# Optimization experiments

Measured on AMD Instinct MI355X. Metric: run time of the kernel, lower is better.

The kernel has to match this reference:

```python
import jax, jax.numpy as jnp
import numpy as np

N = 100000
E = 1600000
IN_F = 256
OUT_F = 128


def setup_inputs() -> dict:
    key = jax.random.key(0)
    k1, k2, k3, k4 = jax.random.split(key, 4)
    x = jax.random.normal(k1, (N, IN_F), dtype=jnp.float32)
    weight = jax.random.normal(k2, (IN_F, OUT_F), dtype=jnp.float32) / np.sqrt(IN_F)
    bias = jax.random.normal(k3, (OUT_F,), dtype=jnp.float32) * 0.01
    edge_index = jax.random.randint(k4, (2, E), 0, N, dtype=jnp.int32)
    return {"x": x, "weight": weight, "bias": bias, "edge_index": edge_index}


def reference(x, weight, bias, edge_index):
    # support = X @ W  -> [N, out]
    support = jnp.matmul(x, weight)
    row, col = edge_index[0], edge_index[1]
    # scatter-add gathered neighbor features: agg[col] += support[row]
    agg = jax.ops.segment_sum(support[row], col, num_segments=N)
    # self term + bias
    return agg + support + bias
```

## Files before the change

### kernel.cpp

```cpp
#include <hip/hip_runtime.h>

#define NUM_NODES 100000
#define IN_F 256
#define OUT_F 128
#define TILE 128
#define NT ((NUM_NODES + TILE - 1) / TILE)
#define NSG 98
#define CHUNK1 4096
#define CHUNK2 4096
#define CAP1 20480
#define SUB2 (CAP1 / CHUNK2)
#define CAP 2560

typedef __attribute__((ext_vector_type(8))) short bf16x8;
typedef __attribute__((ext_vector_type(4))) float f32x4;

__device__ inline unsigned short f2bf(float f) {
    unsigned u = __float_as_uint(f);
    u = (u + 0x7FFFu + ((u >> 16) & 1u)) >> 16;
    return (unsigned short)u;
}
__device__ inline float bf_lo(unsigned int u) { return __uint_as_float(u << 16); }
__device__ inline float bf_hi(unsigned int u) { return __uint_as_float(u & 0xFFFF0000u); }

__global__ __launch_bounds__(256) void convert_wt_kernel(
    const float* __restrict__ w, unsigned short* __restrict__ wt)
{
    int g = blockIdx.x * 256 + threadIdx.x;
    int k = g >> 7, n = g & 127;
    wt[n * 256 + k] = f2bf(w[g]);
}

__global__ __launch_bounds__(512) void gemm_mfma_kernel(
    const float* __restrict__ x, const unsigned short* __restrict__ wt,
    unsigned short* __restrict__ support_h)
{
    __shared__ unsigned short WT[128][264];

    const int tid = threadIdx.x;
    const uint4* src = reinterpret_cast<const uint4*>(wt);
#pragma unroll
    for (int i = 0; i < 8; ++i) {
        int j = tid + i * 512;
        int r = j >> 5;
        int c = (j & 31) << 3;
        *reinterpret_cast<uint4*>(&WT[r][c]) = src[j];
    }
    __syncthreads();

    const int wave = tid >> 6;
    const int lane = tid & 63;
    const int q = lane >> 4;
    const int r16 = lane & 15;
    const int strip_row = blockIdx.x * 128 + wave * 16;

    int arow = strip_row + r16;
    if (arow >= NUM_NODES) arow = NUM_NODES - 1;
    const float* xrow = x + (size_t)arow * IN_F + q * 8;

    f32x4 acc[8];
#pragma unroll
    for (int n = 0; n < 8; ++n) acc[n] = (f32x4){0.f, 0.f, 0.f, 0.f};

#pragma unroll
    for (int half = 0; half < 2; ++half) {
        float4 a[8];
#pragma unroll
        for (int g = 0; g < 4; ++g) {
            const float* p = xrow + half * 128 + g * 32;
            a[g * 2]     = *reinterpret_cast<const float4*>(p);
            a[g * 2 + 1] = *reinterpret_cast<const float4*>(p + 4);
        }
#pragma unroll
        for (int g = 0; g < 4; ++g) {
            const int k0 = half * 128 + g * 32;
            bf16x8 af;
            af[0] = (short)f2bf(a[g * 2].x);
            af[1] = (short)f2bf(a[g * 2].y);
            af[2] = (short)f2bf(a[g * 2].z);
            af[3] = (short)f2bf(a[g * 2].w);
            af[4] = (short)f2bf(a[g * 2 + 1].x);
            af[5] = (short)f2bf(a[g * 2 + 1].y);
            af[6] = (short)f2bf(a[g * 2 + 1].z);
            af[7] = (short)f2bf(a[g * 2 + 1].w);
#pragma unroll
            for (int n = 0; n < 8; ++n) {
                bf16x8 bfr = *reinterpret_cast<const bf16x8*>(
                    &WT[n * 16 + r16][k0 + q * 8]);
                acc[n] = __builtin_amdgcn_mfma_f32_16x16x32_bf16(
                    af, bfr, acc[n], 0, 0, 0);
            }
        }
    }

#pragma unroll
    for (int n = 0; n < 8; ++n) {
#pragma unroll
        for (int rr = 0; rr < 4; ++rr) {
            int grow = strip_row + q * 4 + rr;
            if (grow < NUM_NODES)
                support_h[(size_t)grow * OUT_F + n * 16 + r16] = f2bf(acc[n][rr]);
        }
    }
}

__global__ __launch_bounds__(256) void sg_split_kernel(
    const int* __restrict__ ei, int E, int* __restrict__ gcur1,
    unsigned int* __restrict__ g1rec)
{
    __shared__ int hist[NSG], base[NSG], gbase[NSG], cur[NSG];
    __shared__ unsigned int sorted[CHUNK1];
    const int t = threadIdx.x;
    const int e0 = blockIdx.x * CHUNK1;

    for (int i = t; i < NSG; i += 256) hist[i] = 0;
    __syncthreads();

#pragma unroll
    for (int i = 0; i < CHUNK1 / 256; ++i) {
        int e = e0 + i * 256 + t;
        if (e < E) atomicAdd(&hist[ei[E + e] >> 10], 1);
    }
    __syncthreads();

    {
        int* scan = (int*)sorted;
        const int i0 = t * 4;
        int v0 = (i0     < NSG) ? hist[i0]     : 0;
        int v1 = (i0 + 1 < NSG) ? hist[i0 + 1] : 0;
        int v2 = (i0 + 2 < NSG) ? hist[i0 + 2] : 0;
        int v3 = (i0 + 3 < NSG) ? hist[i0 + 3] : 0;
        int s = v0 + v1 + v2 + v3;
        scan[t] = s;
        __syncthreads();
        for (int off = 1; off < 256; off <<= 1) {
            int v = scan[t];
            int u = (t >= off) ? scan[t - off] : 0;
            __syncthreads();
            scan[t] = v + u;
            __syncthreads();
        }
        int ex = scan[t] - s;
        if (i0     < NSG) base[i0]     = ex;
        if (i0 + 1 < NSG) base[i0 + 1] = ex + v0;
        if (i0 + 2 < NSG) base[i0 + 2] = ex + v0 + v1;
        if (i0 + 3 < NSG) base[i0 + 3] = ex + v0 + v1 + v2;
    }
    __syncthreads();

    if (t < NSG) {
        int n = hist[t];
        gbase[t] = n ? atomicAdd(&gcur1[t], n) : 0;
        cur[t] = base[t];
    }
    __syncthreads();

#pragma unroll
    for (int i = 0; i < CHUNK1 / 256; ++i) {
        int e = e0 + i * 256 + t;
        if (e < E) {
            int row = ei[e], col = ei[E + e];
            int b = col >> 10;
            int pos = atomicAdd(&cur[b], 1);
            sorted[pos] = ((unsigned)row << 10) | (unsigned)(col & 1023);
        }
    }
    __syncthreads();

    const int w = t >> 6, l = t & 63;
    for (int b = w; b < NSG; b += 4) {
        int n = hist[b];
        if (!n) continue;
        int gb = gbase[b], bb = base[b];
        for (int j = l; j < n; j += 64) {
            int dst = gb + j;
            if (dst < CAP1)
                g1rec[(size_t)b * CAP1 + dst] = sorted[bb + j];
        }
    }
}

__global__ __launch_bounds__(256) void tile_split2_kernel(
    const unsigned int* __restrict__ g1rec, const int* __restrict__ gcur1,
    int* __restrict__ gcursor, unsigned int* __restrict__ brec)
{
    const int sg  = blockIdx.x / SUB2;
    const int sub = blockIdx.x % SUB2;
    int cnt = gcur1[sg];
    if (cnt > CAP1) cnt = CAP1;
    const int s0 = sub * CHUNK2;
    if (s0 >= cnt) return;
    const int csize = min(CHUNK2, cnt - s0);
    const unsigned int* src = g1rec + (size_t)sg * CAP1 + s0;

    __shared__ int hist2[32], cur2[32];
    __shared__ int nb[8], bbase[8], gbase2[8];
    __shared__ unsigned int sorted2[CHUNK2];

    const int t = threadIdx.x;
    const int lane = t & 63;
    const int wid = t >> 6;

    if (t < 32) hist2[t] = 0;
    __syncthreads();

#pragma unroll
    for (int i = 0; i < CHUNK2 / 256; ++i) {
        int idx = i * 256 + t;
        if (idx < csize) {
            unsigned r = src[idx];
            atomicAdd(&hist2[wid * 8 + ((r >> 7) & 7)], 1);
        }
    }
    __syncthreads();

    if (t < 8) {
        int run = 0;
#pragma unroll
        for (int w2 = 0; w2 < 4; ++w2) {
            cur2[w2 * 8 + t] = run;
            run += hist2[w2 * 8 + t];
        }
        nb[t] = run;
    }
    __syncthreads();
    if (t == 0) {
        int run = 0;
#pragma unroll
        for (int b = 0; b < 8; ++b) { bbase[b] = run; run += nb[b]; }
    }
    if (t < 8 && nb[t] > 0)
        gbase2[t] = atomicAdd(&gcursor[sg * 8 + t], nb[t]);
    __syncthreads();

#pragma unroll
    for (int i = 0; i < CHUNK2 / 256; ++i) {
        int idx = i * 256 + t;
        if (idx < csize) {
            unsigned r = src[idx];
            int b = (r >> 7) & 7;
            int pos = atomicAdd(&cur2[wid * 8 + b], 1);
            sorted2[bbase[b] + pos] = ((r >> 10) << 7) | (r & 127u);
        }
    }
    __syncthreads();

    for (int b = wid; b < 8; b += 4) {
        int n = nb[b];
        if (!n) continue;
        int gb = gbase2[b], bb = bbase[b];
        size_t tb = (size_t)(sg * 8 + b) * CAP;
        for (int j = lane; j < n; j += 64) {
            int dst = gb + j;
            if (dst < CAP)
                brec[tb + dst] = sorted2[bb + j];
        }
    }
}

__global__ __launch_bounds__(512) void tile_sort_agg_kernel(
    const unsigned int* __restrict__ support_bf,
    const unsigned int* __restrict__ brec,
    const int* __restrict__ gcursor,
    const float* __restrict__ bias,
    float* __restrict__ out)
{
    __shared__ unsigned int recs[CAP];
    __shared__ int srow[CAP];
    __shared__ int hist[128], off[128], cur[128];

    const int tid = threadIdx.x;
    const int lane = tid & 63;
    const int wid = tid >> 6;
    const int node0 = blockIdx.x << 7;

    float accx[16], accy[16];
#pragma unroll
    for (int li = 0; li < 16; ++li) { accx[li] = 0.f; accy[li] = 0.f; }

    int cnt = gcursor[blockIdx.x];
    if (cnt > CAP) cnt = CAP;
    const unsigned int* tb = brec + (size_t)blockIdx.x * CAP;

    if (tid < 128) hist[tid] = 0;
    __syncthreads();

    for (int i = tid; i < cnt; i += 512) {
        unsigned r = tb[i];
        recs[i] = r;
        atomicAdd(&hist[r & 127], 1);
    }
    __syncthreads();

    if (wid == 0) {
        int h0 = hist[2 * lane];
        int h1 = hist[2 * lane + 1];
        int s = h0 + h1;
        int sc = s;
#pragma unroll
        for (int d = 1; d < 64; d <<= 1) {
            int t2 = __shfl_up(sc, d);
            if (lane >= d) sc += t2;
        }
        int ex = sc - s;
        off[2 * lane]     = ex;
        off[2 * lane + 1] = ex + h0;
        cur[2 * lane]     = ex;
        cur[2 * lane + 1] = ex + h0;
    }
    __syncthreads();

    for (int i = tid; i < cnt; i += 512) {
        unsigned r = recs[i];
        int pos = atomicAdd(&cur[r & 127], 1);
        srow[pos] = (int)(r >> 7);
    }
    __syncthreads();

#pragma unroll
    for (int li = 0; li < 16; ++li) {
        const int c = li * 8 + wid;
        int j = off[c];
        const int jend = j + hist[c];
        float ax = accx[li], ay = accy[li];
        for (; j + 7 < jend; j += 8) {
            int r0 = srow[j],     r1 = srow[j + 1];
            int r2 = srow[j + 2], r3 = srow[j + 3];
            int r4 = srow[j + 4], r5 = srow[j + 5];
            int r6 = srow[j + 6], r7 = srow[j + 7];
            unsigned u0 = support_bf[(size_t)r0 * 64 + lane];
            unsigned u1 = support_bf[(size_t)r1 * 64 + lane];
            unsigned u2 = support_bf[(size_t)r2 * 64 + lane];
            unsigned u3 = support_bf[(size_t)r3 * 64 + lane];
            unsigned u4 = support_bf[(size_t)r4 * 64 + lane];
            unsigned u5 = support_bf[(size_t)r5 * 64 + lane];
            unsigned u6 = support_bf[(size_t)r6 * 64 + lane];
            unsigned u7 = support_bf[(size_t)r7 * 64 + lane];
            ax += bf_lo(u0); ay += bf_hi(u0);
            ax += bf_lo(u1); ay += bf_hi(u1);
            ax += bf_lo(u2); ay += bf_hi(u2);
            ax += bf_lo(u3); ay += bf_hi(u3);
            ax += bf_lo(u4); ay += bf_hi(u4);
            ax += bf_lo(u5); ay += bf_hi(u5);
            ax += bf_lo(u6); ay += bf_hi(u6);
            ax += bf_lo(u7); ay += bf_hi(u7);
        }
        for (; j + 3 < jend; j += 4) {
            int r0 = srow[j],     r1 = srow[j + 1];
            int r2 = srow[j + 2], r3 = srow[j + 3];
            unsigned u0 = support_bf[(size_t)r0 * 64 + lane];
            unsigned u1 = support_bf[(size_t)r1 * 64 + lane];
            unsigned u2 = support_bf[(size_t)r2 * 64 + lane];
            unsigned u3 = support_bf[(size_t)r3 * 64 + lane];
            ax += bf_lo(u0); ay += bf_hi(u0);
            ax += bf_lo(u1); ay += bf_hi(u1);
            ax += bf_lo(u2); ay += bf_hi(u2);
            ax += bf_lo(u3); ay += bf_hi(u3);
        }
        for (; j < jend; ++j) {
            unsigned u0 = support_bf[(size_t)srow[j] * 64 + lane];
            ax += bf_lo(u0); ay += bf_hi(u0);
        }
        accx[li] = ax; accy[li] = ay;
    }

    const int nrows = min(TILE, NUM_NODES - node0);
    float2 bi = *reinterpret_cast<const float2*>(bias + lane * 2);
#pragma unroll
    for (int li = 0; li < 16; ++li) {
        const int c = li * 8 + wid;
        if (c < nrows) {
            const int nd = node0 + c;
            unsigned s = support_bf[(size_t)nd * 64 + lane];
            float2 o = {accx[li] + bf_lo(s) + bi.x,
                        accy[li] + bf_hi(s) + bi.y};
            *reinterpret_cast<float2*>(out + (size_t)nd * OUT_F + lane * 2) = o;
        }
    }
}

extern "C" void kernel_launch(void* const* d_in, const int* in_sizes, int n_in,
                              void* d_out, int out_size, void* d_ws, size_t ws_size,
                              hipStream_t stream) {
    const float* x    = (const float*)d_in[0];
    const float* w    = (const float*)d_in[1];
    const float* bias = (const float*)d_in[2];
    const int*   ei   = (const int*)d_in[3];
    float* out = (float*)d_out;
    const int E = in_sizes[3] / 2;
    const int N = NUM_NODES;

    unsigned int* support_bf = (unsigned int*)d_ws;
    unsigned short* wt_bf = (unsigned short*)(support_bf + (size_t)N * 64);
    int* gcursor = (int*)(wt_bf + 128 * 256);
    int* gcur1   = gcursor + 1024;
    unsigned int* g1rec = (unsigned int*)(gcur1 + 128);
    unsigned int* brec  = g1rec + (size_t)NSG * CAP1;

    convert_wt_kernel<<<128, 256, 0, stream>>>(w, wt_bf);
    gemm_mfma_kernel<<<(N + 127) / 128, 512, 0, stream>>>(
        x, wt_bf, (unsigned short*)support_bf);

    hipMemsetAsync(gcursor, 0, (1024 + 128) * sizeof(int), stream);
    sg_split_kernel<<<(E + CHUNK1 - 1) / CHUNK1, 256, 0, stream>>>(
        ei, E, gcur1, g1rec);
    tile_split2_kernel<<<NSG * SUB2, 256, 0, stream>>>(
        g1rec, gcur1, gcursor, brec);

    tile_sort_agg_kernel<<<NT, 512, 0, stream>>>(
        support_bf, brec, gcursor, bias, out);
}
```

Baseline: 141.4 us.

## Fuse GEMM and first-level edge split into one interleaved-role kernel

Merges the MFMA GEMM kernel and the first edge bucketing kernel into a single launch whose blocks alternate between GEMM and split roles, sharing LDS through a union. The independent stages can overlap on the GPU and one launch is removed. The split part now uses 512 threads, a 2048-edge chunk and a wave-shuffle scan. The aggregation gather loop is also unrolled from 8 to 16 loads to raise memory-level parallelism, at the cost of more registers. The larger LDS footprint of the union may reduce occupancy for the split blocks.

Result: slower. 166.8 us (+18.0%).

```diff
diff --git a/kernel.cpp b/kernel.cpp
--- a/kernel.cpp
+++ b/kernel.cpp
@@ -6,7 +6,7 @@
 #define TILE 128
 #define NT ((NUM_NODES + TILE - 1) / TILE)
 #define NSG 98
-#define CHUNK1 4096
+#define CHUNK1 2048
 #define CHUNK2 4096
 #define CAP1 20480
 #define SUB2 (CAP1 / CHUNK2)
@@ -31,151 +31,150 @@
     wt[n * 256 + k] = f2bf(w[g]);
 }
 
-__global__ __launch_bounds__(512) void gemm_mfma_kernel(
+struct ShmGemm { unsigned short WT[128][264]; };
+struct ShmSplit {
+    int hist[128], base[128], gbase[128], cur[128];
+    unsigned int sorted[CHUNK1];
+};
+union ShmK1 { ShmGemm g; ShmSplit s; };
+
+__global__ __launch_bounds__(512) void gemm_split_kernel(
     const float* __restrict__ x, const unsigned short* __restrict__ wt,
-    unsigned short* __restrict__ support_h)
+    unsigned short* __restrict__ support_h,
+    const int* __restrict__ ei, int E,
+    int* __restrict__ gcur1, unsigned int* __restrict__ g1rec,
+    int nG, int nS)
 {
-    __shared__ unsigned short WT[128][264];
-
+    __shared__ ShmK1 shm;
     const int tid = threadIdx.x;
-    const uint4* src = reinterpret_cast<const uint4*>(wt);
-#pragma unroll
-    for (int i = 0; i < 8; ++i) {
-        int j = tid + i * 512;
-        int r = j >> 5;
-        int c = (j & 31) << 3;
-        *reinterpret_cast<uint4*>(&WT[r][c]) = src[j];
-    }
-    __syncthreads();
-
-    const int wave = tid >> 6;
     const int lane = tid & 63;
-    const int q = lane >> 4;
-    const int r16 = lane & 15;
-    const int strip_row = blockIdx.x * 128 + wave * 16;
-
-    int arow = strip_row + r16;
-    if (arow >= NUM_NODES) arow = NUM_NODES - 1;
-    const float* xrow = x + (size_t)arow * IN_F + q * 8;
-
-    f32x4 acc[8];
-#pragma unroll
-    for (int n = 0; n < 8; ++n) acc[n] = (f32x4){0.f, 0.f, 0.f, 0.f};
-
-#pragma unroll
-    for (int half = 0; half < 2; ++half) {
-        float4 a[8];
-#pragma unroll
-        for (int g = 0; g < 4; ++g) {
-            const float* p = xrow + half * 128 + g * 32;
-            a[g * 2]     = *reinterpret_cast<const float4*>(p);
-            a[g * 2 + 1] = *reinterpret_cast<const float4*>(p + 4);
-        }
-#pragma unroll
-        for (int g = 0; g < 4; ++g) {
-            const int k0 = half * 128 + g * 32;
-            bf16x8 af;
-            af[0] = (short)f2bf(a[g * 2].x);
-            af[1] = (short)f2bf(a[g * 2].y);
-            af[2] = (short)f2bf(a[g * 2].z);
-            af[3] = (short)f2bf(a[g * 2].w);
-            af[4] = (short)f2bf(a[g * 2 + 1].x);
-            af[5] = (short)f2bf(a[g * 2 + 1].y);
-            af[6] = (short)f2bf(a[g * 2 + 1].z);
-            af[7] = (short)f2bf(a[g * 2 + 1].w);
-#pragma unroll
-            for (int n = 0; n < 8; ++n) {
-                bf16x8 bfr = *reinterpret_cast<const bf16x8*>(
-                    &WT[n * 16 + r16][k0 + q * 8]);
-                acc[n] = __builtin_amdgcn_mfma_f32_16x16x32_bf16(
-                    af, bfr, acc[n], 0, 0, 0);
-            }
-        }
-    }
-
-#pragma unroll
-    for (int n = 0; n < 8; ++n) {
-#pragma unroll
-        for (int rr = 0; rr < 4; ++rr) {
-            int grow = strip_row + q * 4 + rr;
-            if (grow < NUM_NODES)
-                support_h[(size_t)grow * OUT_F + n * 16 + r16] = f2bf(acc[n][rr]);
-        }
-    }
-}
-
-__global__ __launch_bounds__(256) void sg_split_kernel(
-    const int* __restrict__ ei, int E, int* __restrict__ gcur1,
-    unsigned int* __restrict__ g1rec)
-{
-    __shared__ int hist[NSG], base[NSG], gbase[NSG], cur[NSG];
-    __shared__ unsigned int sorted[CHUNK1];
-    const int t = threadIdx.x;
-    const int e0 = blockIdx.x * CHUNK1;
-
-    for (int i = t; i < NSG; i += 256) hist[i] = 0;
-    __syncthreads();
-
-#pragma unroll
-    for (int i = 0; i < CHUNK1 / 256; ++i) {
-        int e = e0 + i * 256 + t;
-        if (e < E) atomicAdd(&hist[ei[E + e] >> 10], 1);
-    }
-    __syncthreads();
-
-    {
-        int* scan = (int*)sorted;
-        const int i0 = t * 4;
-        int v0 = (i0     < NSG) ? hist[i0]     : 0;
-        int v1 = (i0 + 1 < NSG) ? hist[i0 + 1] : 0;
-        int v2 = (i0 + 2 < NSG) ? hist[i0 + 2] : 0;
-        int v3 = (i0 + 3 < NSG) ? hist[i0 + 3] : 0;
-        int s = v0 + v1 + v2 + v3;
-        scan[t] = s;
+    const int wid = tid >> 6;
+
+    int bid = blockIdx.x;
+    int nmin = nG < nS ? nG : nS;
+    int role, idx;
+    if (bid < 2 * nmin) { role = bid & 1; idx = bid >> 1; }
+    else { role = (nG < nS) ? 1 : 0; idx = bid - 2 * nmin + nmin; }
+
+    if (role == 0) {
+        const uint4* src = reinterpret_cast<const uint4*>(wt);
+#pragma unroll
+        for (int i = 0; i < 8; ++i) {
+            int j = tid + i * 512;
+            int r = j >> 5;
+            int c = (j & 31) << 3;
+            *reinterpret_cast<uint4*>(&shm.g.WT[r][c]) = src[j];
+        }
         __syncthreads();
-        for (int off = 1; off < 256; off <<= 1) {
-            int v = scan[t];
-            int u = (t >= off) ? scan[t - off] : 0;
-            __syncthreads();
-            scan[t] = v + u;
-            __syncthreads();
-        }
-        int ex = scan[t] - s;
-        if (i0     < NSG) base[i0]     = ex;
-        if (i0 + 1 < NSG) base[i0 + 1] = ex + v0;
-        if (i0 + 2 < NSG) base[i0 + 2] = ex + v0 + v1;
-        if (i0 + 3 < NSG) base[i0 + 3] = ex + v0 + v1 + v2;
-    }
-    __syncthreads();
-
-    if (t < NSG) {
-        int n = hist[t];
-        gbase[t] = n ? atomicAdd(&gcur1[t], n) : 0;
-        cur[t] = base[t];
-    }
-    __syncthreads();
-
-#pragma unroll
-    for (int i = 0; i < CHUNK1 / 256; ++i) {
-        int e = e0 + i * 256 + t;
-        if (e < E) {
-            int row = ei[e], col = ei[E + e];
-            int b = col >> 10;
-            int pos = atomicAdd(&cur[b], 1);
-            sorted[pos] = ((unsigned)row << 10) | (unsigned)(col & 1023);
-        }
-    }
-    __syncthreads();
-
-    const int w = t >> 6, l = t & 63;
-    for (int b = w; b < NSG; b += 4) {
-        int n = hist[b];
-        if (!n) continue;
-        int gb = gbase[b], bb = base[b];
-        for (int j = l; j < n; j += 64) {
-            int dst = gb + j;
-            if (dst < CAP1)
-                g1rec[(size_t)b * CAP1 + dst] = sorted[bb + j];
+
+        const int q = lane >> 4;
+        const int r16 = lane & 15;
+        const int strip_row = idx * 128 + wid * 16;
+
+        int arow = strip_row + r16;
+        if (arow >= NUM_NODES) arow = NUM_NODES - 1;
+        const float* xrow = x + (size_t)arow * IN_F + q * 8;
+
+        f32x4 acc[8];
+#pragma unroll
+        for (int n = 0; n < 8; ++n) acc[n] = (f32x4){0.f, 0.f, 0.f, 0.f};
+
+#pragma unroll
+        for (int half = 0; half < 2; ++half) {
+            float4 a[8];
+#pragma unroll
+            for (int g = 0; g < 4; ++g) {
+                const float* p = xrow + half * 128 + g * 32;
+                a[g * 2]     = *reinterpret_cast<const float4*>(p);
+                a[g * 2 + 1] = *reinterpret_cast<const float4*>(p + 4);
+            }
+#pragma unroll
+            for (int g = 0; g < 4; ++g) {
+                const int k0 = half * 128 + g * 32;
+                bf16x8 af;
+                af[0] = (short)f2bf(a[g * 2].x);
+                af[1] = (short)f2bf(a[g * 2].y);
+                af[2] = (short)f2bf(a[g * 2].z);
+                af[3] = (short)f2bf(a[g * 2].w);
+                af[4] = (short)f2bf(a[g * 2 + 1].x);
+                af[5] = (short)f2bf(a[g * 2 + 1].y);
+                af[6] = (short)f2bf(a[g * 2 + 1].z);
+                af[7] = (short)f2bf(a[g * 2 + 1].w);
+#pragma unroll
+                for (int n = 0; n < 8; ++n) {
+                    bf16x8 bfr = *reinterpret_cast<const bf16x8*>(
+                        &shm.g.WT[n * 16 + r16][k0 + q * 8]);
+                    acc[n] = __builtin_amdgcn_mfma_f32_16x16x32_bf16(
+                        af, bfr, acc[n], 0, 0, 0);
+                }
+            }
+        }
+
+#pragma unroll
+        for (int n = 0; n < 8; ++n) {
+#pragma unroll
+            for (int rr = 0; rr < 4; ++rr) {
+                int grow = strip_row + q * 4 + rr;
+                if (grow < NUM_NODES)
+                    support_h[(size_t)grow * OUT_F + n * 16 + r16] =
+                        f2bf(acc[n][rr]);
+            }
+        }
+    } else {
+        const int e0 = idx * CHUNK1;
+
+        if (tid < 128) shm.s.hist[tid] = 0;
+        __syncthreads();
+
+#pragma unroll
+        for (int i = 0; i < CHUNK1 / 512; ++i) {
+            int e = e0 + i * 512 + tid;
+            if (e < E) atomicAdd(&shm.s.hist[ei[E + e] >> 10], 1);
+        }
+        __syncthreads();
+
+        if (wid == 0) {
+            int h0 = shm.s.hist[2 * lane];
+            int h1 = shm.s.hist[2 * lane + 1];
+            int s = h0 + h1;
+            int sc = s;
+#pragma unroll
+            for (int d = 1; d < 64; d <<= 1) {
+                int t2 = __shfl_up(sc, d);
+                if (lane >= d) sc += t2;
+            }
+            int ex = sc - s;
+            shm.s.base[2 * lane]     = ex;      shm.s.cur[2 * lane]     = ex;
+            shm.s.base[2 * lane + 1] = ex + h0; shm.s.cur[2 * lane + 1] = ex + h0;
+            shm.s.gbase[2 * lane] =
+                h0 ? atomicAdd(&gcur1[2 * lane], h0) : 0;
+            shm.s.gbase[2 * lane + 1] =
+                h1 ? atomicAdd(&gcur1[2 * lane + 1], h1) : 0;
+        }
+        __syncthreads();
+
+#pragma unroll
+        for (int i = 0; i < CHUNK1 / 512; ++i) {
+            int e = e0 + i * 512 + tid;
+            if (e < E) {
+                int row = ei[e], col = ei[E + e];
+                int b = col >> 10;
+                int pos = atomicAdd(&shm.s.cur[b], 1);
+                shm.s.sorted[pos] =
+                    ((unsigned)row << 10) | (unsigned)(col & 1023);
+            }
+        }
+        __syncthreads();
+
+        for (int b = wid; b < NSG; b += 8) {
+            int n = shm.s.hist[b];
+            if (!n) continue;
+            int gb = shm.s.gbase[b], bb = shm.s.base[b];
+            for (int j = lane; j < n; j += 64) {
+                int dst = gb + j;
+                if (dst < CAP1)
+                    g1rec[(size_t)b * CAP1 + dst] = shm.s.sorted[bb + j];
+            }
         }
     }
 }
@@ -303,10 +302,8 @@
             if (lane >= d) sc += t2;
         }
         int ex = sc - s;
-        off[2 * lane]     = ex;
-        off[2 * lane + 1] = ex + h0;
-        cur[2 * lane]     = ex;
-        cur[2 * lane + 1] = ex + h0;
+        off[2 * lane]     = ex;      cur[2 * lane]     = ex;
+        off[2 * lane + 1] = ex + h0; cur[2 * lane + 1] = ex + h0;
     }
     __syncthreads();
 
@@ -323,11 +320,15 @@
         int j = off[c];
         const int jend = j + hist[c];
         float ax = accx[li], ay = accy[li];
-        for (; j + 7 < jend; j += 8) {
-            int r0 = srow[j],     r1 = srow[j + 1];
-            int r2 = srow[j + 2], r3 = srow[j + 3];
-            int r4 = srow[j + 4], r5 = srow[j + 5];
-            int r6 = srow[j + 6], r7 = srow[j + 7];
+        for (; j + 15 < jend; j += 16) {
+            int r0 = srow[j],      r1 = srow[j + 1];
+            int r2 = srow[j + 2],  r3 = srow[j + 3];
+            int r4 = srow[j + 4],  r5 = srow[j + 5];
+            int r6 = srow[j + 6],  r7 = srow[j + 7];
+            int r8 = srow[j + 8],  r9 = srow[j + 9];
+            int rA = srow[j + 10], rB = srow[j + 11];
+            int rC = srow[j + 12], rD = srow[j + 13];
+            int rE = srow[j + 14], rF = srow[j + 15];
             unsigned u0 = support_bf[(size_t)r0 * 64 + lane];
             unsigned u1 = support_bf[(size_t)r1 * 64 + lane];
             unsigned u2 = support_bf[(size_t)r2 * 64 + lane];
@@ -336,6 +337,14 @@
             unsigned u5 = support_bf[(size_t)r5 * 64 + lane];
             unsigned u6 = support_bf[(size_t)r6 * 64 + lane];
             unsigned u7 = support_bf[(size_t)r7 * 64 + lane];
+            unsigned u8 = support_bf[(size_t)r8 * 64 + lane];
+            unsigned u9 = support_bf[(size_t)r9 * 64 + lane];
+            unsigned uA = support_bf[(size_t)rA * 64 + lane];
+            unsigned uB = support_bf[(size_t)rB * 64 + lane];
+            unsigned uC = support_bf[(size_t)rC * 64 + lane];
+            unsigned uD = support_bf[(size_t)rD * 64 + lane];
+            unsigned uE = support_bf[(size_t)rE * 64 + lane];
+            unsigned uF = support_bf[(size_t)rF * 64 + lane];
             ax += bf_lo(u0); ay += bf_hi(u0);
             ax += bf_lo(u1); ay += bf_hi(u1);
             ax += bf_lo(u2); ay += bf_hi(u2);
@@ -344,6 +353,14 @@
             ax += bf_lo(u5); ay += bf_hi(u5);
             ax += bf_lo(u6); ay += bf_hi(u6);
             ax += bf_lo(u7); ay += bf_hi(u7);
+            ax += bf_lo(u8); ay += bf_hi(u8);
+            ax += bf_lo(u9); ay += bf_hi(u9);
+            ax += bf_lo(uA); ay += bf_hi(uA);
+            ax += bf_lo(uB); ay += bf_hi(uB);
+            ax += bf_lo(uC); ay += bf_hi(uC);
+            ax += bf_lo(uD); ay += bf_hi(uD);
+            ax += bf_lo(uE); ay += bf_hi(uE);
+            ax += bf_lo(uF); ay += bf_hi(uF);
         }
         for (; j + 3 < jend; j += 4) {
             int r0 = srow[j],     r1 = srow[j + 1];
@@ -397,13 +414,15 @@
     unsigned int* g1rec = (unsigned int*)(gcur1 + 128);
     unsigned int* brec  = g1rec + (size_t)NSG * CAP1;
 
+    const int nG = (N + 127) / 128;
+    const int nS = (E + CHUNK1 - 1) / CHUNK1;
+
     convert_wt_kernel<<<128, 256, 0, stream>>>(w, wt_bf);
-    gemm_mfma_kernel<<<(N + 127) / 128, 512, 0, stream>>>(
-        x, wt_bf, (unsigned short*)support_bf);
-
     hipMemsetAsync(gcursor, 0, (1024 + 128) * sizeof(int), stream);
-    sg_split_kernel<<<(E + CHUNK1 - 1) / CHUNK1, 256, 0, stream>>>(
-        ei, E, gcur1, g1rec);
+
+    gemm_split_kernel<<<nG + nS, 512, 0, stream>>>(
+        x, wt_bf, (unsigned short*)support_bf, ei, E, gcur1, g1rec, nG, nS);
+
     tile_split2_kernel<<<NSG * SUB2, 256, 0, stream>>>(
         g1rec, gcur1, gcursor, brec);
 
```
